# Kernel tuning notes

Measured on AMD Instinct MI355X. Metric: run time of the kernel, lower is better.

Reference implementation:

```python
import jax, jax.numpy as jnp
import numpy as np

# Power-of-two, per-tensor, signed fake quantization (brevitas CustomQuant):
# scale = 2^ceil(log2(max|x| / int_max)), restrict POWER_OF_TWO, stats MAX,
# signed, narrow_range=False -> int range [-2^(b-1), 2^(b-1)-1].
# Weights use ROUND, activations use FLOOR (CustomSignedActQuant).

def _fake_quant(x, bits, rnd_fn):
    int_max = 2.0 ** (bits - 1) - 1.0   # 127 for 8-bit
    int_min = -(2.0 ** (bits - 1))      # -128
    max_abs = jnp.max(jnp.abs(x))
    scale = 2.0 ** jnp.ceil(jnp.log2(jnp.maximum(max_abs, 1e-10) / int_max))
    q = jnp.clip(rnd_fn(x / scale), int_min, int_max) * scale
    # straight-through estimator (quant-dequant forward, identity backward)
    return x + jax.lax.stop_gradient(q - x)


def setup_inputs() -> dict:
    key = jax.random.key(0)
    ks = jax.random.split(key, 7)
    B, C, H, W, P = 16, 728, 64, 64, 728
    x = jax.random.normal(ks[0], (B, C, H, W), jnp.float32)
    w_dw = jax.random.normal(ks[1], (C, 1, 3, 3), jnp.float32) * 0.1   # depthwise, groups=C
    w_pw = jax.random.normal(ks[2], (P, C, 1, 1), jnp.float32) * 0.05  # pointwise 1x1
    gamma = 1.0 + 0.1 * jax.random.normal(ks[3], (C,), jnp.float32)
    beta = 0.1 * jax.random.normal(ks[4], (C,), jnp.float32)
    run_mean = 0.1 * jax.random.normal(ks[5], (C,), jnp.float32)
    run_var = 0.5 + jax.random.uniform(ks[6], (C,), jnp.float32)
    return {"x": x, "w_dw": w_dw, "w_pw": w_pw, "gamma": gamma,
            "beta": beta, "run_mean": run_mean, "run_var": run_var}


def reference(x, w_dw, w_pw, gamma, beta, run_mean, run_var):
    C = x.shape[1]
    eps = 1e-5
    # fixed_padding: kernel=3, dilation=1 -> pad_total=2 -> (1,1) each side
    xp = jnp.pad(x, ((0, 0), (0, 0), (1, 1), (1, 1)))
    # quantized depthwise conv (groups = inplanes)
    wq = _fake_quant(w_dw, 8, jnp.round)
    y = jax.lax.conv_general_dilated(
        xp, wq, window_strides=(1, 1), padding='VALID',
        dimension_numbers=('NCHW', 'OIHW', 'NCHW'),
        feature_group_count=C)
    # BatchNorm2d (eval mode, running stats)
    inv = gamma / jnp.sqrt(run_var + eps)                # [C]
    y = y * inv[:, None, None] + (beta - run_mean * inv)[:, None, None]
    # quantized identity on activations (FLOOR)
    y = _fake_quant(y, 8, jnp.floor)
    # quantized pointwise 1x1 conv
    wpq = _fake_quant(w_pw, 8, jnp.round)
    out = jnp.einsum('bchw,oc->bohw', y, wpq[:, :, 0, 0])
    return out
```

## Files before the change

### kernel.cpp

```cpp
#include <hip/hip_runtime.h>

#define C_IN 728
#define NB   16
#define HH   64
#define WW   64
#define HW   4096
#define KPAD 736
#define MPAD 768

typedef __bf16 bf16x8 __attribute__((ext_vector_type(8)));
typedef float  f32x4  __attribute__((ext_vector_type(4)));
typedef unsigned short us8 __attribute__((ext_vector_type(8)));

__device__ __forceinline__ float p2scale(unsigned bits, float int_max) {
    float ma = __uint_as_float(bits);
    float v = fmaxf(ma, 1e-10f) / int_max;
    int e; float m = frexpf(v, &e);
    if (m == 0.5f) e -= 1;
    return ldexpf(1.0f, e);
}

__global__ void init_slots(unsigned* slots) {
    if (threadIdx.x < 3) slots[threadIdx.x] = 0u;
}

__device__ __forceinline__ float block_max(float v) {
    #pragma unroll
    for (int off = 32; off; off >>= 1) v = fmaxf(v, __shfl_down(v, off));
    __shared__ float red[4];
    int lane = threadIdx.x & 63, wv = threadIdx.x >> 6;
    if (lane == 0) red[wv] = v;
    __syncthreads();
    return fmaxf(fmaxf(red[0], red[1]), fmaxf(red[2], red[3]));
}

__global__ __launch_bounds__(256) void maxabs_kernel(const float* __restrict__ p, int n,
                                                     unsigned* slot) {
    float v = 0.f;
    for (int i = blockIdx.x * 256 + threadIdx.x; i < n; i += gridDim.x * 256)
        v = fmaxf(v, fabsf(p[i]));
    float m = block_max(v);
    if (threadIdx.x == 0)
        atomicMax(slot, __float_as_uint(m));
}

__global__ __launch_bounds__(256) void quant_dw(const float* __restrict__ w,
                                                float* __restrict__ wq,
                                                const unsigned* __restrict__ slots) {
    int i = blockIdx.x * 256 + threadIdx.x;
    if (i >= C_IN * 9) return;
    float s = p2scale(slots[0], 127.f);
    float k = fminf(fmaxf(rintf(w[i] / s), -128.f), 127.f);
    wq[i] = k * s;
}

__global__ __launch_bounds__(256) void dwconv_bn(const float* __restrict__ x,
                                                 const float* __restrict__ wq,
                                                 const float* __restrict__ gamma,
                                                 const float* __restrict__ beta,
                                                 const float* __restrict__ rmean,
                                                 const float* __restrict__ rvar,
                                                 float* __restrict__ y,
                                                 float* __restrict__ partial) {
    __shared__ __align__(16) float tile[HW];
    const int c = blockIdx.x, b = blockIdx.y, t = threadIdx.x;
    const float* xp = x + ((size_t)b * C_IN + c) * HW;

    const float4* xv = (const float4*)xp;
    float4* tv = (float4*)tile;
    #pragma unroll
    for (int i = 0; i < 4; ++i) tv[t + i * 256] = xv[t + i * 256];

    float wk[9];
    #pragma unroll
    for (int j = 0; j < 9; ++j) wk[j] = wq[c * 9 + j];
    const float inv  = gamma[c] / sqrtf(rvar[c] + 1e-5f);
    const float bias = beta[c] - rmean[c] * inv;
    __syncthreads();

    float* yp = y + ((size_t)b * C_IN + c) * HW;
    float vmax = 0.f;
    #pragma unroll
    for (int i = 0; i < 16; ++i) {
        const int p = t + i * 256;
        const int h = p >> 6, wc = p & 63;
        float acc = 0.f;
        #pragma unroll
        for (int dh = -1; dh <= 1; ++dh) {
            const int hh = h + dh;
            if ((unsigned)hh < (unsigned)HH) {
                const int base = hh << 6;
                if (wc > 0)  acc += tile[base + wc - 1] * wk[(dh + 1) * 3 + 0];
                acc += tile[base + wc] * wk[(dh + 1) * 3 + 1];
                if (wc < 63) acc += tile[base + wc + 1] * wk[(dh + 1) * 3 + 2];
            }
        }
        const float val = acc * inv + bias;
        yp[p] = val;
        vmax = fmaxf(vmax, fabsf(val));
    }
    const float m = block_max(vmax);
    if (t == 0) partial[b * C_IN + c] = m;
}

__global__ __launch_bounds__(256) void reduce_partial(const float* __restrict__ p, int n,
                                                      unsigned* __restrict__ slot) {
    float v = 0.f;
    for (int i = threadIdx.x; i < n; i += 256) v = fmaxf(v, p[i]);
    float m = block_max(v);
    if (threadIdx.x == 0) *slot = __float_as_uint(m);
}

__global__ __launch_bounds__(256) void quant_wpw(const float* __restrict__ w,
                                                 unsigned short* __restrict__ wq,
                                                 const unsigned* __restrict__ slots) {
    int i = blockIdx.x * 256 + threadIdx.x;
    if (i >= MPAD * KPAD) return;
    int o = i / KPAD, c = i % KPAD;
    float k = 0.f;
    if (o < C_IN && c < C_IN) {
        float s = p2scale(slots[1], 127.f);
        k = fminf(fmaxf(rintf(w[o * C_IN + c] / s), -128.f), 127.f);
    }
    wq[i] = (unsigned short)(__float_as_uint(k) >> 16);
}

__global__ __launch_bounds__(256) void transpose_quant_y(const float* __restrict__ y,
                                                         unsigned short* __restrict__ yq,
                                                         const unsigned* __restrict__ slots) {
    __shared__ __align__(16) float tile[128 * 36];
    const int t   = threadIdx.x;
    const int hw0 = blockIdx.x * 32;
    const int c0  = blockIdx.y * 128;
    const int b   = blockIdx.z;
    const float inv_s = 1.0f / p2scale(slots[2], 127.f);

    #pragma unroll
    for (int i = 0; i < 4; ++i) {
        const int gi = i * 256 + t;
        const int cl = gi >> 3, g = gi & 7;
        const int c  = c0 + cl;
        float4 v = make_float4(0.f, 0.f, 0.f, 0.f);
        if (c < C_IN)
            v = *(const float4*)(y + ((size_t)(b * C_IN + c)) * HW + hw0 + g * 4);
        const int gp = g ^ ((cl >> 3) & 7);
        *(float4*)(tile + cl * 36 + gp * 4) = v;
    }
    __syncthreads();

    #pragma unroll
    for (int it = 0; it < 2; ++it) {
        const int hw_r = (t >> 4) + it * 16;
        const int c8   = t & 15;
        const int c_out = c0 + c8 * 8;
        if (c_out < KPAD) {
            us8 pack;
            #pragma unroll
            for (int j = 0; j < 8; ++j) {
                const int cl = c8 * 8 + j;
                const int gp = (hw_r >> 2) ^ (c8 & 7);
                const float v = tile[cl * 36 + gp * 4 + (hw_r & 3)];
                const float k = fminf(fmaxf(floorf(v * inv_s), -128.f), 127.f);
                pack[j] = (unsigned short)(__float_as_uint(k) >> 16);
            }
            *(us8*)(yq + ((size_t)b * HW + hw0 + hw_r) * KPAD + c_out) = pack;
        }
    }
}

__global__ __launch_bounds__(256) void gemm_kernel(const unsigned short* __restrict__ Wq,
                                                   const unsigned short* __restrict__ Yq,
                                                   float* __restrict__ out,
                                                   const unsigned* __restrict__ slots) {
    __shared__ __align__(16) unsigned short As[128 * 32];
    __shared__ __align__(16) unsigned short Bs[128 * 32];
    const int t = threadIdx.x;
    const int w = t >> 6, l = t & 63;
    const int r = l & 15, q = l >> 4;
    const int wr = w >> 1, wc = w & 1;
    const int m0 = blockIdx.y * 128;
    const int n0 = blockIdx.x * 128;
    const int b  = blockIdx.z;

    const unsigned short* Ag = Wq + (size_t)m0 * KPAD;
    const unsigned short* Bg = Yq + ((size_t)b * HW + n0) * KPAD;

    const int srow = t >> 2;
    const int sko  = ((t & 3) ^ ((t >> 3) & 3)) * 8;
    const int swr  = (r >> 1) & 3;

    f32x4 acc[4][4];
    #pragma unroll
    for (int i = 0; i < 4; ++i)
        #pragma unroll
        for (int j = 0; j < 4; ++j) acc[i][j] = (f32x4){0.f, 0.f, 0.f, 0.f};

    for (int k0 = 0; k0 < KPAD; k0 += 32) {
        __builtin_amdgcn_global_load_lds(
            (const __attribute__((address_space(1))) void*)(Ag + (size_t)srow * KPAD + k0 + sko),
            (__attribute__((address_space(3))) void*)(As + w * 512), 16, 0, 0);
        __builtin_amdgcn_global_load_lds(
            (const __attribute__((address_space(1))) void*)(Ag + (size_t)(64 + srow) * KPAD + k0 + sko),
            (__attribute__((address_space(3))) void*)(As + 2048 + w * 512), 16, 0, 0);
        __builtin_amdgcn_global_load_lds(
            (const __attribute__((address_space(1))) void*)(Bg + (size_t)srow * KPAD + k0 + sko),
            (__attribute__((address_space(3))) void*)(Bs + w * 512), 16, 0, 0);
        __builtin_amdgcn_global_load_lds(
            (const __attribute__((address_space(1))) void*)(Bg + (size_t)(64 + srow) * KPAD + k0 + sko),
            (__attribute__((address_space(3))) void*)(Bs + 2048 + w * 512), 16, 0, 0);
        __syncthreads();

        bf16x8 af[4], bfr[4];
        #pragma unroll
        for (int fm = 0; fm < 4; ++fm)
            af[fm] = *(const bf16x8*)(As + (wr * 64 + fm * 16 + r) * 32 + ((q ^ swr)) * 8);
        #pragma unroll
        for (int fn = 0; fn < 4; ++fn)
            bfr[fn] = *(const bf16x8*)(Bs + (wc * 64 + fn * 16 + r) * 32 + ((q ^ swr)) * 8);
        #pragma unroll
        for (int fm = 0; fm < 4; ++fm)
            #pragma unroll
            for (int fn = 0; fn < 4; ++fn)
                acc[fm][fn] = __builtin_amdgcn_mfma_f32_16x16x32_bf16(
                    af[fm], bfr[fn], acc[fm][fn], 0, 0, 0);
        __syncthreads();
    }

    const float stot = p2scale(slots[1], 127.f) * p2scale(slots[2], 127.f);
    #pragma unroll
    for (int fm = 0; fm < 4; ++fm) {
        int o = m0 + wr * 64 + fm * 16 + q * 4;
        #pragma unroll
        for (int fn = 0; fn < 4; ++fn) {
            int hw = n0 + wc * 64 + fn * 16 + r;
            float* op = out + ((size_t)b * C_IN + o) * HW + hw;
            #pragma unroll
            for (int reg = 0; reg < 4; ++reg) {
                if (o + reg < C_IN) op[(size_t)reg * HW] = acc[fm][fn][reg] * stot;
            }
        }
    }
}

extern "C" void kernel_launch(void* const* d_in, const int* in_sizes, int n_in,
                              void* d_out, int out_size, void* d_ws, size_t ws_size,
                              hipStream_t stream) {
    const float* x     = (const float*)d_in[0];
    const float* w_dw  = (const float*)d_in[1];
    const float* w_pw  = (const float*)d_in[2];
    const float* gamma = (const float*)d_in[3];
    const float* beta  = (const float*)d_in[4];
    const float* rmean = (const float*)d_in[5];
    const float* rvar  = (const float*)d_in[6];
    float* out = (float*)d_out;

    char* ws = (char*)d_ws;
    unsigned*       slots = (unsigned*)ws;
    float*          wq_dw = (float*)(ws + 256);
    unsigned short* Wq    = (unsigned short*)(ws + 26624);
    float*          y     = (float*)(ws + 1157120);
    unsigned short* Yq    = (unsigned short*)(ws + 191997952);
    float*          partial = (float*)(ws + 191997952);

    init_slots<<<dim3(1), dim3(64), 0, stream>>>(slots);
    maxabs_kernel<<<dim3(4), dim3(256), 0, stream>>>(w_dw, C_IN * 9, slots + 0);
    maxabs_kernel<<<dim3(64), dim3(256), 0, stream>>>(w_pw, C_IN * C_IN, slots + 1);
    quant_dw<<<dim3((C_IN * 9 + 255) / 256), dim3(256), 0, stream>>>(w_dw, wq_dw, slots);
    dwconv_bn<<<dim3(C_IN, NB), dim3(256), 0, stream>>>(
        x, wq_dw, gamma, beta, rmean, rvar, y, partial);
    reduce_partial<<<dim3(1), dim3(256), 0, stream>>>(partial, NB * C_IN, slots + 2);
    quant_wpw<<<dim3((MPAD * KPAD + 255) / 256), dim3(256), 0, stream>>>(w_pw, Wq, slots);
    transpose_quant_y<<<dim3(HW / 32, KPAD / 128 + 1, NB), dim3(256), 0, stream>>>(y, Yq, slots);
    gemm_kernel<<<dim3(HW / 128, MPAD / 128, NB), dim3(256), 0, stream>>>(Wq, Yq, out, slots);
}
```

Baseline: 581.6 us.

## Use zero-padded LDS tile with register-blocked 16-wide rows in depthwise conv

The depthwise conv kernel now stores the input plane in a zero-padded 66x68 LDS tile, which removes the per-tap boundary branches. Each thread computes 16 consecutive outputs of one row from vector-loaded row segments held in registers, so each LDS value is reused across neighbouring taps. Outputs are written as float4 stores. The cost is higher register pressure from the 16 accumulators and 20-element row buffers, plus some extra LDS space and scalar LDS writes during staging.

```diff
diff --git a/kernel.cpp b/kernel.cpp
--- a/kernel.cpp
+++ b/kernel.cpp
@@ -7,6 +7,7 @@
 #define HW   4096
 #define KPAD 736
 #define MPAD 768
+#define PROW 68
 
 typedef __bf16 bf16x8 __attribute__((ext_vector_type(8)));
 typedef float  f32x4  __attribute__((ext_vector_type(4)));
@@ -62,14 +63,23 @@
                                                  const float* __restrict__ rvar,
                                                  float* __restrict__ y,
                                                  float* __restrict__ partial) {
-    __shared__ __align__(16) float tile[HW];
+    __shared__ __align__(16) float tile[66 * PROW];
     const int c = blockIdx.x, b = blockIdx.y, t = threadIdx.x;
     const float* xp = x + ((size_t)b * C_IN + c) * HW;
 
+    if (t < 136) { int hr = t / PROW, cc = t - hr * PROW; tile[hr * 65 * PROW + cc] = 0.f; }
+    { int hr = 1 + (t & 63); int g = t >> 6; int cc = (g == 0) ? 0 : (64 + g);
+      tile[hr * PROW + cc] = 0.f; }
+
     const float4* xv = (const float4*)xp;
-    float4* tv = (float4*)tile;
-    #pragma unroll
-    for (int i = 0; i < 4; ++i) tv[t + i * 256] = xv[t + i * 256];
+    #pragma unroll
+    for (int i = 0; i < 4; ++i) {
+        const int idx4 = t + i * 256;
+        const float4 v = xv[idx4];
+        const int h = idx4 >> 4, c4 = idx4 & 15;
+        float* dst = tile + (h + 1) * PROW + 4 * c4 + 1;
+        dst[0] = v.x; dst[1] = v.y; dst[2] = v.z; dst[3] = v.w;
+    }
 
     float wk[9];
     #pragma unroll
@@ -78,26 +88,36 @@
     const float bias = beta[c] - rmean[c] * inv;
     __syncthreads();
 
-    float* yp = y + ((size_t)b * C_IN + c) * HW;
+    const int r = t >> 2, qt = t & 3;
+    float acc[16];
+    #pragma unroll
+    for (int j = 0; j < 16; ++j) acc[j] = 0.f;
+
+    #pragma unroll
+    for (int dr = 0; dr < 3; ++dr) {
+        const float* rowp = tile + (r + dr) * PROW + 16 * qt;
+        float rv[20];
+        #pragma unroll
+        for (int i = 0; i < 5; ++i)
+            *(f32x4*)(rv + 4 * i) = *(const f32x4*)(rowp + 4 * i);
+        const float w0 = wk[dr * 3 + 0], w1 = wk[dr * 3 + 1], w2 = wk[dr * 3 + 2];
+        #pragma unroll
+        for (int j = 0; j < 16; ++j)
+            acc[j] += rv[j] * w0 + rv[j + 1] * w1 + rv[j + 2] * w2;
+    }
+
+    float* yp = y + ((size_t)b * C_IN + c) * HW + r * WW + 16 * qt;
     float vmax = 0.f;
     #pragma unroll
-    for (int i = 0; i < 16; ++i) {
-        const int p = t + i * 256;
-        const int h = p >> 6, wc = p & 63;
-        float acc = 0.f;
-        #pragma unroll
-        for (int dh = -1; dh <= 1; ++dh) {
-            const int hh = h + dh;
-            if ((unsigned)hh < (unsigned)HH) {
-                const int base = hh << 6;
-                if (wc > 0)  acc += tile[base + wc - 1] * wk[(dh + 1) * 3 + 0];
-                acc += tile[base + wc] * wk[(dh + 1) * 3 + 1];
-                if (wc < 63) acc += tile[base + wc + 1] * wk[(dh + 1) * 3 + 2];
-            }
-        }
-        const float val = acc * inv + bias;
-        yp[p] = val;
-        vmax = fmaxf(vmax, fabsf(val));
+    for (int j4 = 0; j4 < 4; ++j4) {
+        float4 o;
+        o.x = acc[4 * j4 + 0] * inv + bias;
+        o.y = acc[4 * j4 + 1] * inv + bias;
+        o.z = acc[4 * j4 + 2] * inv + bias;
+        o.w = acc[4 * j4 + 3] * inv + bias;
+        vmax = fmaxf(vmax, fmaxf(fmaxf(fabsf(o.x), fabsf(o.y)),
+                                 fmaxf(fabsf(o.z), fabsf(o.w))));
+        ((float4*)yp)[j4] = o;
     }
     const float m = block_max(vmax);
     if (t == 0) partial[b * C_IN + c] = m;
```

Measured after the change: 575.1 us. About the same (-1.1%).
